# Kernel tuning notes

Hardware: AMD Instinct MI355X
Metric: run time of the kernel (lower is better)

## Reference

```python
import jax, jax.numpy as jnp
import numpy as np

EMB_DIM = 1024
NUM_HEADS = 16
HEAD_DIM = EMB_DIM // NUM_HEADS  # 64
B, S = 2, 2048


def setup_inputs() -> dict:
    key = jax.random.key(0)
    ks = jax.random.split(key, 9)
    scale = 1.0 / np.sqrt(EMB_DIM)
    return {
        "query": jax.random.normal(ks[0], (B, S, EMB_DIM), dtype=jnp.float32),
        "Wq": jax.random.normal(ks[1], (EMB_DIM, EMB_DIM), dtype=jnp.float32) * scale,
        "bq": jax.random.normal(ks[2], (EMB_DIM,), dtype=jnp.float32) * 0.01,
        "Wk": jax.random.normal(ks[3], (EMB_DIM, EMB_DIM), dtype=jnp.float32) * scale,
        "bk": jax.random.normal(ks[4], (EMB_DIM,), dtype=jnp.float32) * 0.01,
        "Wv": jax.random.normal(ks[5], (EMB_DIM, EMB_DIM), dtype=jnp.float32) * scale,
        "bv": jax.random.normal(ks[6], (EMB_DIM,), dtype=jnp.float32) * 0.01,
        "Wo": jax.random.normal(ks[7], (EMB_DIM, EMB_DIM), dtype=jnp.float32) * scale,
        "bo": jax.random.normal(ks[8], (EMB_DIM,), dtype=jnp.float32) * 0.01,
    }


def reference(query, Wq, bq, Wk, bk, Wv, bv, Wo, bo):
    # Self-attention path (key_value=None, mask=None in the original forward).
    b, s, _ = query.shape
    # torch nn.Linear: y = x @ W.T + b
    def proj(x, W, bias):
        y = jnp.einsum('bse,fe->bsf', x, W) + bias
        # [B,S,E] -> [B,H,S,D]
        return y.reshape(b, s, NUM_HEADS, HEAD_DIM).transpose(0, 2, 1, 3)

    q = proj(query, Wq, bq)
    k = proj(query, Wk, bk)
    v = proj(query, Wv, bv)

    scores = jnp.einsum('bhqd,bhkd->bhqk', q, k) / np.sqrt(HEAD_DIM).astype(np.float32)
    attn = jax.nn.softmax(scores, axis=-1)  # [B,H,S,S]
    out = jnp.einsum('bhqk,bhkd->bhqd', attn, v)
    out = out.transpose(0, 2, 1, 3).reshape(b, s, EMB_DIM)
    return jnp.einsum('bse,fe->bsf', out, Wo) + bo
```

## Files before the change

kernel.cpp:

```cpp
#include <hip/hip_runtime.h>
#include <hip/hip_bf16.h>

using bf16x4 = __attribute__((ext_vector_type(4))) short;
using short8 = __attribute__((ext_vector_type(8))) short;
using f32x4  = __attribute__((ext_vector_type(4))) float;
using u32x2  = __attribute__((ext_vector_type(2))) unsigned;

__device__ __forceinline__ short f2bf(float f) {
  unsigned u = __builtin_bit_cast(unsigned, f);
  u = (u + 0x7fffu + ((u >> 16) & 1u)) >> 16;
  return (short)u;
}
__device__ __forceinline__ float bf2f(short s) {
  unsigned u = ((unsigned)(unsigned short)s) << 16;
  return __builtin_bit_cast(float, u);
}
__device__ __forceinline__ unsigned pk2(float a, float b) {
  __hip_bfloat162 h = __float22bfloat162_rn(make_float2(a, b));
  unsigned u; __builtin_memcpy(&u, &h, 4);
  return u;
}
__device__ __forceinline__ void gload16(const short* g, short* l) {
  __builtin_amdgcn_global_load_lds(
      (const __attribute__((address_space(1))) unsigned int*)g,
      (__attribute__((address_space(3))) unsigned int*)l, 16, 0, 0);
}

constexpr int E  = 1024;
constexpr int SL = 2048;
constexpr int NB = 2;
constexpr int NH = 16;
constexpr int M  = NB * SL;

__global__ __launch_bounds__(256) void convert_kernel(
    const float* __restrict__ X,  const float* __restrict__ Wq,
    const float* __restrict__ Wk, const float* __restrict__ Wv,
    const float* __restrict__ Wo, short* __restrict__ out)
{
  const size_t i8 = ((size_t)blockIdx.x * 256 + threadIdx.x) * 8;
  const float* src;
  if (i8 < (size_t)(4u << 20)) {
    src = X + i8;
  } else {
    size_t r = i8 - (size_t)(4u << 20);
    int wi = (int)(r >> 20);
    size_t off = r & ((1u << 20) - 1);
    src = (wi == 0 ? Wq : wi == 1 ? Wk : wi == 2 ? Wv : Wo) + off;
  }
  f32x4 a = *(const f32x4*)src;
  f32x4 b = *(const f32x4*)(src + 4);
  short hb[8];
#pragma unroll
  for (int e = 0; e < 4; ++e) { hb[e] = f2bf(a[e]); hb[4 + e] = f2bf(b[e]); }
  *(short8*)(out + i8) = *(short8*)hb;
}

template <int TM, int TN, bool SPLIT, bool OUTF32, bool FUSEV>
__global__ __launch_bounds__(256) void gemm_kernel(
    const short* __restrict__ A0, const short* __restrict__ A1, const short* __restrict__ A2,
    const short* __restrict__ Al_,
    const short* __restrict__ W0, const short* __restrict__ W1, const short* __restrict__ W2,
    const float* __restrict__ b0, const float* __restrict__ b1, const float* __restrict__ b2,
    void* __restrict__ Y0, void* __restrict__ Y1, void* __restrict__ Y2,
    float s0, float s1, float s2, int ld0, int ld1, int ld2)
{
  constexpr int BK = 64;
  constexpr int RA = TM / 32;
  constexpr int RB = TN / 32;
  constexpr int WM = TM / 2, WN = TN / 2;
  constexpr int NI = WM / 16, NJ = WN / 16;
  __shared__ alignas(16) short As[TM * BK];
  __shared__ alignas(16) short Als[SPLIT ? TM * BK : 8];
  __shared__ alignas(16) short Bs[TN * BK];
  const int t = threadIdx.x;
  const int l = t & 63;
  const int w = t >> 6;
  const int c = l & 15;
  const int g = l >> 4;
  const int z = blockIdx.z;
  const short* Ap = (z == 0) ? A0 : (z == 1) ? A1 : A2;
  const short* Wp = (z == 0) ? W0 : (z == 1) ? W1 : W2;
  const float* bp = (z == 0) ? b0 : (z == 1) ? b1 : b2;
  void* Yp        = (z == 0) ? Y0 : (z == 1) ? Y1 : Y2;
  const float sc  = (z == 0) ? s0 : (z == 1) ? s1 : s2;
  const int ldY   = (z == 0) ? ld0 : (z == 1) ? ld1 : ld2;
  const bool vtr  = FUSEV && (z == 2);
  const int m0 = (vtr ? blockIdx.y : blockIdx.x) * TM;
  const int n0 = (vtr ? blockIdx.x : blockIdx.y) * TN;

  const short* gA[RA]; short* lA[RA];
  const short* gB[RB]; short* lB[RB];
  const short* gL[SPLIT ? RA : 1]; short* lL[SPLIT ? RA : 1];
#pragma unroll
  for (int r = 0; r < RA; ++r) {
    const int cc = r * 256 + t;
    gA[r] = Ap + (size_t)(m0 + (cc >> 3)) * E + (cc & 7) * 8;
    lA[r] = As + (size_t)(r * 256 + (t & ~63)) * 8;
    if constexpr (SPLIT) {
      gL[r] = Al_ + (size_t)(m0 + (cc >> 3)) * E + (cc & 7) * 8;
      lL[r] = Als + (size_t)(r * 256 + (t & ~63)) * 8;
    }
  }
#pragma unroll
  for (int r = 0; r < RB; ++r) {
    const int cc = r * 256 + t;
    gB[r] = Wp + (size_t)(n0 + (cc >> 3)) * E + (cc & 7) * 8;
    lB[r] = Bs + (size_t)(r * 256 + (t & ~63)) * 8;
  }

  const int wm = (w >> 1) * WM;
  const int wn = (w & 1) * WN;
  f32x4 acc[NI][NJ] = {};

  for (int k0 = 0; k0 < E; k0 += BK) {
#pragma unroll
    for (int r = 0; r < RA; ++r) gload16(gA[r] + k0, lA[r]);
    if constexpr (SPLIT) {
#pragma unroll
      for (int r = 0; r < RA; ++r) gload16(gL[r] + k0, lL[r]);
    }
#pragma unroll
    for (int r = 0; r < RB; ++r) gload16(gB[r] + k0, lB[r]);
    __syncthreads();
#pragma unroll
    for (int kk = 0; kk < 2; ++kk) {
      short8 ah[NI], alo[SPLIT ? NI : 1], bfr[NJ];
#pragma unroll
      for (int i = 0; i < NI; ++i) {
        ah[i] = *(const short8*)&As[(wm + i * 16 + c) * BK + kk * 32 + g * 8];
        if constexpr (SPLIT)
          alo[i] = *(const short8*)&Als[(wm + i * 16 + c) * BK + kk * 32 + g * 8];
      }
#pragma unroll
      for (int j = 0; j < NJ; ++j)
        bfr[j] = *(const short8*)&Bs[(wn + j * 16 + c) * BK + kk * 32 + g * 8];
#pragma unroll
      for (int i = 0; i < NI; ++i)
#pragma unroll
        for (int j = 0; j < NJ; ++j) {
          acc[i][j] = __builtin_amdgcn_mfma_f32_16x16x32_bf16(ah[i], bfr[j], acc[i][j], 0, 0, 0);
          if constexpr (SPLIT)
            acc[i][j] = __builtin_amdgcn_mfma_f32_16x16x32_bf16(alo[i], bfr[j], acc[i][j], 0, 0, 0);
        }
    }
    __syncthreads();
  }

#pragma unroll
  for (int j = 0; j < NJ; ++j) {
    const int col = n0 + wn + j * 16 + c;
    const float bcol = vtr ? 0.f : bp[col];
#pragma unroll
    for (int i = 0; i < NI; ++i) {
      const int rowb = m0 + wm + i * 16 + g * 4;
#pragma unroll
      for (int r = 0; r < 4; ++r) {
        const int row = rowb + r;
        const float bias = vtr ? bp[row] : bcol;
        const float v = (acc[i][j][r] + bias) * sc;
        if (OUTF32) ((float*)Yp)[(size_t)row * ldY + col] = v;
        else        ((short*)Yp)[(size_t)row * ldY + col] = f2bf(v);
      }
    }
  }
}

__global__ __launch_bounds__(512) void flash_kernel(
    const short* __restrict__ Qm, const short* __restrict__ Km,
    const short* __restrict__ VTm, short* __restrict__ Oh)
{
  __shared__ alignas(16) short Ks[64][72];
  __shared__ alignas(16) short Vt[64][72];
  __shared__ alignas(16) short Pl[8][16][72];
  const int t = threadIdx.x;
  const int l = t & 63;
  const int w = t >> 6;
  const int c = l & 15;
  const int g = l >> 4;
  const int q0 = blockIdx.x * 128;
  const int bh = (int)blockIdx.y;
  const int b = bh >> 4;
  const int h = bh & 15;
  const size_t baseK = (size_t)b * SL * E + h * 64;
  const size_t baseV = (size_t)(h * 64) * M + (size_t)b * SL;

  short8 aq[2];
  {
    const short* qp = Qm + baseK + (size_t)(q0 + w * 16 + c) * E + g * 8;
    aq[0] = *(const short8*)qp;
    aq[1] = *(const short8*)(qp + 32);
  }

  f32x4 lacc = {0.f, 0.f, 0.f, 0.f};
  f32x4 acc_o[4] = {};

  const int srow = t >> 3, sseg = t & 7;
  const short* gK = Km + baseK + (size_t)srow * E + sseg * 8;
  const short* gV = VTm + baseV + (size_t)srow * M + sseg * 8;

  short8 kreg = *(const short8*)gK;
  short8 vreg = *(const short8*)gV;

  constexpr int NT = SL / 64;
  for (int kt = 0; kt < NT; ++kt) {
    __syncthreads();
    *(short8*)&Ks[srow][sseg * 8] = kreg;
    *(short8*)&Vt[srow][sseg * 8] = vreg;
    __syncthreads();
    if (kt + 1 < NT) {
      kreg = *(const short8*)(gK + (size_t)(kt + 1) * 64 * E);
      vreg = *(const short8*)(gV + (kt + 1) * 64);
    }

    f32x4 st[4] = {};
#pragma unroll
    for (int j = 0; j < 4; ++j)
#pragma unroll
      for (int kc = 0; kc < 2; ++kc) {
        short8 kf = *(const short8*)&Ks[j * 16 + c][kc * 32 + g * 8];
        st[j] = __builtin_amdgcn_mfma_f32_16x16x32_bf16(kf, aq[kc], st[j], 0, 0, 0);
      }

#pragma unroll
    for (int j = 0; j < 4; ++j) {
      f32x4 p;
#pragma unroll
      for (int r = 0; r < 4; ++r) p[r] = __builtin_amdgcn_exp2f(st[j][r]);
      lacc += p;
      u32x2 pk = {pk2(p[0], p[1]), pk2(p[2], p[3])};
      *(u32x2*)&Pl[w][c][j * 16 + g * 4] = pk;
    }
    short8 ap[2];
    ap[0] = *(const short8*)&Pl[w][c][g * 8];
    ap[1] = *(const short8*)&Pl[w][c][32 + g * 8];

#pragma unroll
    for (int j = 0; j < 4; ++j)
#pragma unroll
      for (int kc = 0; kc < 2; ++kc) {
        short8 vf = *(const short8*)&Vt[j * 16 + c][kc * 32 + g * 8];
        acc_o[j] = __builtin_amdgcn_mfma_f32_16x16x32_bf16(vf, ap[kc], acc_o[j], 0, 0, 0);
      }
  }

  float s = lacc[0] + lacc[1] + lacc[2] + lacc[3];
  s += __shfl_xor(s, 16);
  s += __shfl_xor(s, 32);
  const float inv = 1.0f / s;

  const int token = q0 + w * 16 + c;
  const size_t obase = ((size_t)b * SL + token) * E + h * 64;
#pragma unroll
  for (int j = 0; j < 4; ++j) {
    u32x2 o2 = {pk2(acc_o[j][0] * inv, acc_o[j][1] * inv),
                pk2(acc_o[j][2] * inv, acc_o[j][3] * inv)};
    *(u32x2*)(Oh + obase + j * 16 + g * 4) = o2;
  }
}

extern "C" void kernel_launch(void* const* d_in, const int* in_sizes, int n_in,
                              void* d_out, int out_size, void* d_ws, size_t ws_size,
                              hipStream_t stream)
{
  const float* X  = (const float*)d_in[0];
  const float* Wq = (const float*)d_in[1];
  const float* bq = (const float*)d_in[2];
  const float* Wk = (const float*)d_in[3];
  const float* bk = (const float*)d_in[4];
  const float* Wv = (const float*)d_in[5];
  const float* bv = (const float*)d_in[6];
  const float* Wo = (const float*)d_in[7];
  const float* bo = (const float*)d_in[8];
  float* out = (float*)d_out;

  const size_t szX = (size_t)M * E;
  const size_t szW = (size_t)E * E;
  short* Xb  = (short*)d_ws;
  short* Wqb = Xb + szX;
  short* Wkb = Wqb + szW;
  short* Wvb = Wkb + szW;
  short* Wob = Wvb + szW;
  short* Qw  = Wob + szW;
  short* Kw  = Qw + szX;
  short* VTw = Kw + szX;

  convert_kernel<<<4096, 256, 0, stream>>>(X, Wq, Wk, Wv, Wo, Xb);

  const float kLog2eOver8 = 0.18033688011112042f;
  dim3 g1(M / 128, E / 128, 3);
  gemm_kernel<128, 128, false, false, true><<<g1, 256, 0, stream>>>(
      Xb, Xb, Wvb, nullptr,
      Wqb, Wkb, Xb,
      bq, bk, bv,
      (void*)Qw, (void*)Kw, (void*)VTw,
      kLog2eOver8, 1.0f, 1.0f, E, E, M);

  dim3 g2(SL / 128, NB * NH);
  flash_kernel<<<g2, 512, 0, stream>>>(Qw, Kw, VTw, Qw );

  dim3 g3(M / 128, E / 64, 1);
  gemm_kernel<128, 64, false, true, false><<<g3, 256, 0, stream>>>(
      Qw, Qw, Qw, nullptr,
      Wob, Wob, Wob,
      bo, bo, bo,
      (void*)out, (void*)out, (void*)out,
      1.0f, 1.0f, 1.0f, E, E, E);
}
```

Before: 226.8 us.

## Double-buffer GEMM LDS tiles with BK=32 prefetch and drop unused split path

The GEMM kernel now keeps two LDS buffers per operand with K-step 32. The loads for the next K tile are issued right after the barrier, so they overlap the MFMA work on the current tile, and one of the two barriers per iteration is removed. The unused SPLIT (hi/lo) path is also deleted. In exchange the K-loop runs twice as many iterations with half the MFMA work per barrier. The global_load_lds prefetch may not be waited on correctly before the next iteration's reads, unless the single barrier covers the async completion.

```diff
diff --git a/kernel.cpp b/kernel.cpp
--- a/kernel.cpp
+++ b/kernel.cpp
@@ -10,10 +10,6 @@
   unsigned u = __builtin_bit_cast(unsigned, f);
   u = (u + 0x7fffu + ((u >> 16) & 1u)) >> 16;
   return (short)u;
-}
-__device__ __forceinline__ float bf2f(short s) {
-  unsigned u = ((unsigned)(unsigned short)s) << 16;
-  return __builtin_bit_cast(float, u);
 }
 __device__ __forceinline__ unsigned pk2(float a, float b) {
   __hip_bfloat162 h = __float22bfloat162_rn(make_float2(a, b));
@@ -55,23 +51,21 @@
   *(short8*)(out + i8) = *(short8*)hb;
 }
 
-template <int TM, int TN, bool SPLIT, bool OUTF32, bool FUSEV>
+template <int TM, int TN, bool OUTF32, bool FUSEV>
 __global__ __launch_bounds__(256) void gemm_kernel(
     const short* __restrict__ A0, const short* __restrict__ A1, const short* __restrict__ A2,
-    const short* __restrict__ Al_,
     const short* __restrict__ W0, const short* __restrict__ W1, const short* __restrict__ W2,
     const float* __restrict__ b0, const float* __restrict__ b1, const float* __restrict__ b2,
     void* __restrict__ Y0, void* __restrict__ Y1, void* __restrict__ Y2,
     float s0, float s1, float s2, int ld0, int ld1, int ld2)
 {
-  constexpr int BK = 64;
-  constexpr int RA = TM / 32;
-  constexpr int RB = TN / 32;
+  constexpr int BK = 32;
+  constexpr int RA = TM / 64;
+  constexpr int RB = TN / 64;
   constexpr int WM = TM / 2, WN = TN / 2;
   constexpr int NI = WM / 16, NJ = WN / 16;
-  __shared__ alignas(16) short As[TM * BK];
-  __shared__ alignas(16) short Als[SPLIT ? TM * BK : 8];
-  __shared__ alignas(16) short Bs[TN * BK];
+  __shared__ alignas(16) short As[2][TM * BK];
+  __shared__ alignas(16) short Bs[2][TN * BK];
   const int t = threadIdx.x;
   const int l = t & 63;
   const int w = t >> 6;
@@ -88,62 +82,52 @@
   const int m0 = (vtr ? blockIdx.y : blockIdx.x) * TM;
   const int n0 = (vtr ? blockIdx.x : blockIdx.y) * TN;
 
-  const short* gA[RA]; short* lA[RA];
-  const short* gB[RB]; short* lB[RB];
-  const short* gL[SPLIT ? RA : 1]; short* lL[SPLIT ? RA : 1];
+  const short* gA[RA]; int oA[RA];
+  const short* gB[RB]; int oB[RB];
 #pragma unroll
   for (int r = 0; r < RA; ++r) {
     const int cc = r * 256 + t;
-    gA[r] = Ap + (size_t)(m0 + (cc >> 3)) * E + (cc & 7) * 8;
-    lA[r] = As + (size_t)(r * 256 + (t & ~63)) * 8;
-    if constexpr (SPLIT) {
-      gL[r] = Al_ + (size_t)(m0 + (cc >> 3)) * E + (cc & 7) * 8;
-      lL[r] = Als + (size_t)(r * 256 + (t & ~63)) * 8;
-    }
+    gA[r] = Ap + (size_t)(m0 + (cc >> 2)) * E + (cc & 3) * 8;
+    oA[r] = (r * 256 + (t & ~63)) * 8;
   }
 #pragma unroll
   for (int r = 0; r < RB; ++r) {
     const int cc = r * 256 + t;
-    gB[r] = Wp + (size_t)(n0 + (cc >> 3)) * E + (cc & 7) * 8;
-    lB[r] = Bs + (size_t)(r * 256 + (t & ~63)) * 8;
-  }
+    gB[r] = Wp + (size_t)(n0 + (cc >> 2)) * E + (cc & 3) * 8;
+    oB[r] = (r * 256 + (t & ~63)) * 8;
+  }
+
+#pragma unroll
+  for (int r = 0; r < RA; ++r) gload16(gA[r], &As[0][oA[r]]);
+#pragma unroll
+  for (int r = 0; r < RB; ++r) gload16(gB[r], &Bs[0][oB[r]]);
 
   const int wm = (w >> 1) * WM;
   const int wn = (w & 1) * WN;
   f32x4 acc[NI][NJ] = {};
+  int cur = 0;
 
   for (int k0 = 0; k0 < E; k0 += BK) {
-#pragma unroll
-    for (int r = 0; r < RA; ++r) gload16(gA[r] + k0, lA[r]);
-    if constexpr (SPLIT) {
-#pragma unroll
-      for (int r = 0; r < RA; ++r) gload16(gL[r] + k0, lL[r]);
-    }
-#pragma unroll
-    for (int r = 0; r < RB; ++r) gload16(gB[r] + k0, lB[r]);
     __syncthreads();
-#pragma unroll
-    for (int kk = 0; kk < 2; ++kk) {
-      short8 ah[NI], alo[SPLIT ? NI : 1], bfr[NJ];
-#pragma unroll
-      for (int i = 0; i < NI; ++i) {
-        ah[i] = *(const short8*)&As[(wm + i * 16 + c) * BK + kk * 32 + g * 8];
-        if constexpr (SPLIT)
-          alo[i] = *(const short8*)&Als[(wm + i * 16 + c) * BK + kk * 32 + g * 8];
-      }
+    if (k0 + BK < E) {
+#pragma unroll
+      for (int r = 0; r < RA; ++r) gload16(gA[r] + k0 + BK, &As[cur ^ 1][oA[r]]);
+#pragma unroll
+      for (int r = 0; r < RB; ++r) gload16(gB[r] + k0 + BK, &Bs[cur ^ 1][oB[r]]);
+    }
+    short8 ah[NI], bfr[NJ];
+#pragma unroll
+    for (int i = 0; i < NI; ++i)
+      ah[i] = *(const short8*)&As[cur][(wm + i * 16 + c) * BK + g * 8];
+#pragma unroll
+    for (int j = 0; j < NJ; ++j)
+      bfr[j] = *(const short8*)&Bs[cur][(wn + j * 16 + c) * BK + g * 8];
+#pragma unroll
+    for (int i = 0; i < NI; ++i)
 #pragma unroll
       for (int j = 0; j < NJ; ++j)
-        bfr[j] = *(const short8*)&Bs[(wn + j * 16 + c) * BK + kk * 32 + g * 8];
-#pragma unroll
-      for (int i = 0; i < NI; ++i)
-#pragma unroll
-        for (int j = 0; j < NJ; ++j) {
-          acc[i][j] = __builtin_amdgcn_mfma_f32_16x16x32_bf16(ah[i], bfr[j], acc[i][j], 0, 0, 0);
-          if constexpr (SPLIT)
-            acc[i][j] = __builtin_amdgcn_mfma_f32_16x16x32_bf16(alo[i], bfr[j], acc[i][j], 0, 0, 0);
-        }
-    }
-    __syncthreads();
+        acc[i][j] = __builtin_amdgcn_mfma_f32_16x16x32_bf16(ah[i], bfr[j], acc[i][j], 0, 0, 0);
+    cur ^= 1;
   }
 
 #pragma unroll
@@ -288,8 +272,8 @@
 
   const float kLog2eOver8 = 0.18033688011112042f;
   dim3 g1(M / 128, E / 128, 3);
-  gemm_kernel<128, 128, false, false, true><<<g1, 256, 0, stream>>>(
-      Xb, Xb, Wvb, nullptr,
+  gemm_kernel<128, 128, false, true><<<g1, 256, 0, stream>>>(
+      Xb, Xb, Wvb,
       Wqb, Wkb, Xb,
       bq, bk, bv,
       (void*)Qw, (void*)Kw, (void*)VTw,
@@ -299,8 +283,8 @@
   flash_kernel<<<g2, 512, 0, stream>>>(Qw, Kw, VTw, Qw );
 
   dim3 g3(M / 128, E / 64, 1);
-  gemm_kernel<128, 64, false, true, false><<<g3, 256, 0, stream>>>(
-      Qw, Qw, Qw, nullptr,
+  gemm_kernel<128, 64, true, false><<<g3, 256, 0, stream>>>(
+      Qw, Qw, Qw,
       Wob, Wob, Wob,
       bo, bo, bo,
       (void*)out, (void*)out, (void*)out,
```

After: 210.4 us. -7.2%, faster.
